# Optimization experiments

Measured on AMD Instinct MI355X. Metric: run time of the kernel, lower is better.

Reference implementation:

```python
import math
import jax, jax.numpy as jnp
import numpy as np

S, M, B, NH, HD = 512, 512, 8, 16, 64  # SentenceLength, MemoryLength, BatchSize, heads, head_size
H = NH * HD   # 1024 hidden
K = M + S     # key length = r_length
LAYERS, TOTAL_LEN = 2, 1536


def setup_inputs() -> dict:
    key = jax.random.key(0)
    ks = jax.random.split(key, 12)
    w = lambda k: jax.random.normal(k, (H, H), jnp.float32) * 0.02
    return {
        "x": jax.random.normal(ks[0], (B, S, H), jnp.float32),
        "rel_pos_emb": jax.random.normal(ks[1], (K, H), jnp.float32),
        "attention_mask": jnp.ones((B, S), jnp.float32),  # unused by the original forward
        "memories": jax.random.normal(ks[2], (LAYERS, B, TOTAL_LEN, H), jnp.float32),
        "Wq": w(ks[3]), "Wke": w(ks[4]), "Wv": w(ks[5]), "Wkr": w(ks[6]),
        "u": jax.random.normal(ks[7], (NH, HD), jnp.float32),
        "v": jax.random.normal(ks[8], (NH, HD), jnp.float32),
        "Wo": w(ks[9]),
        "bo": jnp.zeros((H,), jnp.float32),
        "layer_num": 0,
        "segment_num": 0,
    }


def rel_shift(bd):
    # Vectorized form of the original per-row loop:
    # row qi keeps bd[qi][qlen-1-qi:] and zero-pads the tail.
    qlen, klen = bd.shape[0], bd.shape[1]
    shift = (qlen - 1) - jnp.arange(qlen)            # [qlen]
    idx = shift[:, None] + jnp.arange(klen)[None, :]  # [qlen, klen]
    valid = (idx < klen)
    idx_c = jnp.minimum(idx, klen - 1)
    out = bd[jnp.arange(qlen)[:, None], idx_c]        # gather along key axis
    return out * valid[:, :, None, None].astype(bd.dtype)


def reference(x, rel_pos_emb, attention_mask, memories, Wq, Wke, Wv, Wkr, u, v, Wo, bo, layer_num, segment_num):
    # memory segment for this layer: [B, M, H]
    sg_m = memories[layer_num, :, segment_num * M:(segment_num + 1) * M, :]
    kvx = jnp.concatenate([sg_m, x], axis=1)          # [B, K, H]
    # Projections, then the original's raw .view() reinterpretation (not a transpose)
    qx = (x.reshape(-1, H) @ Wq).reshape(S, B, NH, HD)
    kx = (kvx.reshape(-1, H) @ Wke).reshape(K, B, NH, HD)
    vx = (kvx.reshape(-1, H) @ Wv).reshape(K, B, NH, HD)
    kr = (rel_pos_emb @ Wkr).reshape(K, NH, HD)
    ac = jnp.einsum('ibnd,jbnd->ijbn', qx + u, kx)    # content score [S,K,B,NH]
    bd = jnp.einsum('ibnd,jnd->ijbn', qx + v, kr)     # position score
    bd = rel_shift(bd)
    att = (ac + bd) / math.sqrt(float(HD))
    att = jax.nn.softmax(att, axis=-1)                # original uses Softmax(dim=-1) on [i,j,b,n]
    out = jnp.einsum('ijbn,jbnd->ibnd', att, vx)      # [S,B,NH,HD]
    out = out.reshape(B, S, H)                        # original's raw contiguous().view()
    out = out @ Wo + bo                               # o_dense (dropout is identity in eval)
    # update_memories_by_layer (no_grad in torch -> stop_gradient here)
    new_mem = memories.at[layer_num, :, segment_num * S + M:(segment_num + 1) * S + M, :].set(
        jax.lax.stop_gradient(out))
    return out, new_mem
```

## Files before the change

### kernel.cpp

```cpp
#include <hip/hip_runtime.h>
#include <hip/hip_bf16.h>

#define OUT_OFF 4194304
#define NM_ELEMS 25165824

typedef __attribute__((ext_vector_type(8))) short short8;
typedef __attribute__((ext_vector_type(4))) float f32x4;

static __device__ __forceinline__ float4 ld4(const float* p) {
  return *reinterpret_cast<const float4*>(p);
}
static __device__ __forceinline__ short bfbits(float f) {
  __hip_bfloat16 h = __float2bfloat16(f);
  return *reinterpret_cast<short*>(&h);
}
static __device__ __forceinline__ void gload16(const void* g, void* l) {
  __builtin_amdgcn_global_load_lds(
      (const __attribute__((address_space(1))) void*)g,
      (__attribute__((address_space(3))) void*)l, 16, 0, 0);
}

__global__ __launch_bounds__(256)
void cw_k(const float* __restrict__ W0, const float* __restrict__ W1,
          const float* __restrict__ W2, const float* __restrict__ W3,
          const float* __restrict__ W4,
          __hip_bfloat16* __restrict__ T0, __hip_bfloat16* __restrict__ T1,
          __hip_bfloat16* __restrict__ T2, __hip_bfloat16* __restrict__ T3,
          __hip_bfloat16* __restrict__ T4)
{
  const float* W; __hip_bfloat16* T;
  switch (blockIdx.z) {
    case 0: W = W0; T = T0; break;
    case 1: W = W1; T = T1; break;
    case 2: W = W2; T = T2; break;
    case 3: W = W3; T = T3; break;
    default: W = W4; T = T4; break;
  }
  __shared__ short S[64][72];
  const int t = threadIdx.x;
  const int n0 = blockIdx.x * 64, k0 = blockIdx.y * 64;
  #pragma unroll
  for (int it = 0; it < 2; ++it) {
    const int kl = (t >> 3) + it * 32;
    const int n8 = (t & 7) * 8;
    const float* src = W + (size_t)(k0 + kl) * 1024 + n0 + n8;
    const float4 f0 = ld4(src), f1 = ld4(src + 4);
    short8 s;
    s[0]=bfbits(f0.x); s[1]=bfbits(f0.y); s[2]=bfbits(f0.z); s[3]=bfbits(f0.w);
    s[4]=bfbits(f1.x); s[5]=bfbits(f1.y); s[6]=bfbits(f1.z); s[7]=bfbits(f1.w);
    *reinterpret_cast<short8*>(&S[kl][n8]) = s;
  }
  __syncthreads();
  #pragma unroll
  for (int it = 0; it < 2; ++it) {
    const int nl = (t >> 3) + it * 32;
    const int k8 = (t & 7) * 8;
    short8 s;
    #pragma unroll
    for (int e = 0; e < 8; ++e) s[e] = S[k8 + e][nl];
    *reinterpret_cast<short8*>((short*)T + (size_t)(n0 + nl) * 1024 + k0 + k8) = s;
  }
}

__global__ __launch_bounds__(256)
void ckvx_k(const float* __restrict__ x, const float* __restrict__ mem,
            const int* __restrict__ lp, const int* __restrict__ sp,
            __hip_bfloat16* __restrict__ Kvx)
{
  const size_t t = (size_t)blockIdx.x * 256 + threadIdx.x;
  const int r = (int)(t >> 7);
  const int c = (int)(t & 127) * 8;
  const int b = r >> 10, j = r & 1023;
  const float* src = (j < 512)
    ? mem + (((size_t)lp[0] * 8 + b) * 1536 + (size_t)sp[0] * 512 + j) * 1024 + c
    : x + ((size_t)b * 512 + (j - 512)) * 1024 + c;
  const float4 f0 = ld4(src), f1 = ld4(src + 4);
  short8 s;
  s[0]=bfbits(f0.x); s[1]=bfbits(f0.y); s[2]=bfbits(f0.z); s[3]=bfbits(f0.w);
  s[4]=bfbits(f1.x); s[5]=bfbits(f1.y); s[6]=bfbits(f1.z); s[7]=bfbits(f1.w);
  *reinterpret_cast<short8*>((short*)Kvx + (size_t)r * 1024 + c) = s;
}

__global__ __launch_bounds__(256)
void crpe_k(const float* __restrict__ R, __hip_bfloat16* __restrict__ Rb)
{
  const size_t t = ((size_t)blockIdx.x * 256 + threadIdx.x) * 8;
  const float4 f0 = ld4(R + t), f1 = ld4(R + t + 4);
  short8 s;
  s[0]=bfbits(f0.x); s[1]=bfbits(f0.y); s[2]=bfbits(f0.z); s[3]=bfbits(f0.w);
  s[4]=bfbits(f1.x); s[5]=bfbits(f1.y); s[6]=bfbits(f1.z); s[7]=bfbits(f1.w);
  *reinterpret_cast<short8*>((short*)Rb + t) = s;
}

template<int MODE>
__global__ __launch_bounds__(256)
void mgemm(const __hip_bfloat16* __restrict__ A,
           const __hip_bfloat16* __restrict__ Wt,
           const float* __restrict__ P0, const float* __restrict__ P1,
           const int* __restrict__ lp, const int* __restrict__ sp,
           __hip_bfloat16* __restrict__ Cb, __hip_bfloat16* __restrict__ Cb2,
           float* __restrict__ C)
{
  __shared__ __align__(16) short As[128 * 64];
  __shared__ __align__(16) short Bs[128 * 64];
  const int tid = threadIdx.x;
  const int w   = tid >> 6;
  const int l   = tid & 63;
  const int l15 = l & 15, lg = l >> 4;
  const int m0 = blockIdx.y * 128;
  const int n0 = blockIdx.x * 128;
  const int wr = (w >> 1) * 64;
  const int wc = (w & 1) * 64;

  f32x4 acc[4][4];
  #pragma unroll
  for (int mi = 0; mi < 4; ++mi)
    #pragma unroll
    for (int ni = 0; ni < 4; ++ni) acc[mi][ni] = (f32x4){0.f, 0.f, 0.f, 0.f};

  const int srow = (l >> 3);
  const int scol = (l & 7) * 8;

  for (int k0 = 0; k0 < 1024; k0 += 64) {
    if (k0) __syncthreads();
    #pragma unroll
    for (int q = 0; q < 4; ++q) {
      const int seg = w * 32 + q * 8;
      const int ra = m0 + seg + srow;
      size_t aoff;
      if (MODE == 4)
        aoff = ((size_t)(ra >> 9) * 1024 + 512 + (ra & 511)) * 1024;
      else
        aoff = (size_t)ra * 1024;
      gload16((const short*)A + aoff + k0 + scol, &As[seg * 64]);
      const int rb = n0 + seg + srow;
      gload16((const short*)Wt + (size_t)rb * 1024 + k0 + scol, &Bs[seg * 64]);
    }
    __syncthreads();
    #pragma unroll
    for (int kk = 0; kk < 2; ++kk) {
      short8 a[4], bf[4];
      #pragma unroll
      for (int mi = 0; mi < 4; ++mi)
        a[mi] = *reinterpret_cast<const short8*>(
            &As[(wr + mi * 16 + l15) * 64 + kk * 32 + lg * 8]);
      #pragma unroll
      for (int ni = 0; ni < 4; ++ni)
        bf[ni] = *reinterpret_cast<const short8*>(
            &Bs[(wc + ni * 16 + l15) * 64 + kk * 32 + lg * 8]);
      #pragma unroll
      for (int mi = 0; mi < 4; ++mi)
        #pragma unroll
        for (int ni = 0; ni < 4; ++ni)
          acc[mi][ni] = __builtin_amdgcn_mfma_f32_16x16x32_bf16(
              a[mi], bf[ni], acc[mi][ni], 0, 0, 0);
    }
  }

  #pragma unroll
  for (int mi = 0; mi < 4; ++mi) {
    const int rbase = m0 + wr + mi * 16 + lg * 4;
    #pragma unroll
    for (int ni = 0; ni < 4; ++ni) {
      const int col = n0 + wc + ni * 16 + l15;
      const int nh = col >> 6, dd = col & 63;
      #pragma unroll
      for (int rr = 0; rr < 4; ++rr) {
        const int row = rbase + rr;
        const float val = acc[mi][ni][rr];
        if (MODE == 3) {
          Cb[(size_t)row * 1024 + col] = __float2bfloat16(val);
        } else if (MODE == 4) {
          const int i = row >> 3, bb = row & 7;
          const size_t o = (((size_t)(bb * 16 + nh) * 512) + i) * 64 + dd;
          Cb [o] = __float2bfloat16(val + P0[col]);
          Cb2[o] = __float2bfloat16(val + P1[col]);
        } else if (MODE == 5) {
          const int j = row >> 3, bb = row & 7;
          Cb[(((size_t)(bb * 16 + nh) * 1024) + j) * 64 + dd] =
              __float2bfloat16(val);
        } else if (MODE == 2) {
          const float o = val + P0[col];
          C[(size_t)row * 1024 + col] = o;
          const int b2 = row >> 9, s2 = row & 511;
          C[OUT_OFF +
            (((size_t)lp[0] * 8 + b2) * 1536 + 512 + (size_t)sp[0] * 512 + s2) *
                1024 + col] = o;
        }
      }
    }
  }
}

__global__ __launch_bounds__(256)
void tr_k(const __hip_bfloat16* __restrict__ VE, __hip_bfloat16* __restrict__ Vt)
{
  __shared__ short T[64][72];
  const int t = threadIdx.x;
  const int j0 = blockIdx.x * 64;
  const int bn = blockIdx.y;
  #pragma unroll
  for (int it = 0; it < 2; ++it) {
    const int jl = (t >> 3) + it * 32;
    const int d8 = (t & 7) * 8;
    *reinterpret_cast<short8*>(&T[jl][d8]) =
        *reinterpret_cast<const short8*>(
            (const short*)VE + ((size_t)bn * 1024 + j0 + jl) * 64 + d8);
  }
  __syncthreads();
  #pragma unroll
  for (int it = 0; it < 2; ++it) {
    const int dl = (t >> 3) + it * 32;
    const int j8 = (t & 7) * 8;
    short8 s;
    #pragma unroll
    for (int e = 0; e < 8; ++e) s[e] = T[j8 + e][dl];
    *reinterpret_cast<short8*>(
        (short*)Vt + ((size_t)bn * 64 + dl) * 1024 + j0 + j8) = s;
  }
}

__global__ __launch_bounds__(512, 1)
void attn2(const __hip_bfloat16* __restrict__ QU, const __hip_bfloat16* __restrict__ QV,
           const __hip_bfloat16* __restrict__ KE, const __hip_bfloat16* __restrict__ Vt,
           const __hip_bfloat16* __restrict__ KR, __hip_bfloat16* __restrict__ Ob)
{
  __shared__ float Lbuf[16*16*33];
  __shared__ __hip_bfloat16 Abuf[16*16*36];

  const int bid = blockIdx.x;
  const int b   = bid & 7;
  const int i0  = (bid >> 3) * 16;
  const int tid = threadIdx.x;
  const int w   = tid >> 6;
  const int l   = tid & 63;
  const int l15 = l & 15;
  const int lg  = l >> 4;

  short8 qu[2][2], qv[2][2];
  #pragma unroll
  for (int hh = 0; hh < 2; ++hh) {
    const int h = 2*w + hh;
    const size_t qb = (((size_t)(b*16 + h) * 512) + i0 + l15) * 64 + lg*8;
    #pragma unroll
    for (int kf = 0; kf < 2; ++kf) {
      qu[hh][kf] = *reinterpret_cast<const short8*>(QU + qb + kf*32);
      qv[hh][kf] = *reinterpret_cast<const short8*>(QV + qb + kf*32);
    }
  }

  f32x4 oacc[2][4];
  #pragma unroll
  for (int hh = 0; hh < 2; ++hh)
    #pragma unroll
    for (int nf = 0; nf < 4; ++nf) oacc[hh][nf] = (f32x4){0.f,0.f,0.f,0.f};

  auto loadKEKR = [&](short8 (&ke)[2][2][2], short8 (&kr)[2][3][2],
                      int j0, int pb) {
    #pragma unroll
    for (int hh = 0; hh < 2; ++hh) {
      const int h = 2*w + hh;
      #pragma unroll
      for (int jf = 0; jf < 2; ++jf)
        #pragma unroll
        for (int kf = 0; kf < 2; ++kf)
          ke[hh][jf][kf] = *reinterpret_cast<const short8*>(
            KE + (((size_t)(b*16 + h) * 1024) + j0 + jf*16 + l15) * 64 + kf*32 + lg*8);
      #pragma unroll
      for (int nf = 0; nf < 3; ++nf)
        #pragma unroll
        for (int kf = 0; kf < 2; ++kf)
          kr[hh][nf][kf] = *reinterpret_cast<const short8*>(
            KR + ((size_t)(pb + nf*16 + l15)) * 1024 + h*64 + kf*32 + lg*8);
    }
  };

  auto body = [&](int jt, short8 (&keC)[2][2][2], short8 (&krC)[2][3][2],
                  short8 (&keN)[2][2][2], short8 (&krN)[2][3][2]) {
    const int j0 = jt * 32;
    const int pb = 496 - i0 + j0;

    f32x4 ac[2][2], tf[2][3];
    #pragma unroll
    for (int hh = 0; hh < 2; ++hh) {
      #pragma unroll
      for (int nf = 0; nf < 3; ++nf) {
        tf[hh][nf] = (f32x4){0,0,0,0};
        #pragma unroll
        for (int kf = 0; kf < 2; ++kf)
          tf[hh][nf] = __builtin_amdgcn_mfma_f32_16x16x32_bf16(
              qv[hh][kf], krC[hh][nf][kf], tf[hh][nf], 0, 0, 0);
      }
      #pragma unroll
      for (int jf = 0; jf < 2; ++jf) {
        ac[hh][jf] = (f32x4){0,0,0,0};
        #pragma unroll
        for (int kf = 0; kf < 2; ++kf)
          ac[hh][jf] = __builtin_amdgcn_mfma_f32_16x16x32_bf16(
              qu[hh][kf], keC[hh][jf][kf], ac[hh][jf], 0, 0, 0);
      }
    }

    loadKEKR(keN, krN, j0 + 32, pb + 32);

    short8 vb[2][4];
    #pragma unroll
    for (int hh = 0; hh < 2; ++hh) {
      const int h = 2*w + hh;
      #pragma unroll
      for (int nf = 0; nf < 4; ++nf)
        vb[hh][nf] = *reinterpret_cast<const short8*>(
          Vt + (((size_t)(b*16 + h) * 64) + nf*16 + l15) * 1024 + j0 + lg*8);
    }

    asm volatile("" ::: "memory");

    #pragma unroll
    for (int hh = 0; hh < 2; ++hh) {
      const int h = 2*w + hh;
      #pragma unroll
      for (int jf = 0; jf < 2; ++jf)
        #pragma unroll
        for (int r = 0; r < 4; ++r) {
          const int ip  = lg*4 + r;
          const int idx = 15 - ip + jf*16 + l15;
          const int nf  = idx >> 4;
          const int Ls  = lg*16 + (idx & 15);
          const float v0 = __shfl(tf[hh][0][r], Ls, 64);
          const float v1 = __shfl(tf[hh][1][r], Ls, 64);
          const float v2 = __shfl(tf[hh][2][r], Ls, 64);
          const float bd = (nf == 0) ? v0 : ((nf == 1) ? v1 : v2);
          Lbuf[(h*16 + ip)*33 + jf*16 + l15] = 0.125f * (ac[hh][jf][r] + bd);
        }
    }
    __syncthreads();

    {
      const int si = tid >> 5, sj = tid & 31;
      float vals[16];
      float m = -3.0e38f;
      #pragma unroll
      for (int n = 0; n < 16; ++n) {
        vals[n] = Lbuf[(n*16 + si)*33 + sj];
        m = fmaxf(m, vals[n]);
      }
      float s = 0.f;
      #pragma unroll
      for (int n = 0; n < 16; ++n) { vals[n] = __expf(vals[n] - m); s += vals[n]; }
      const float rinv = 1.0f / s;
      #pragma unroll
      for (int n = 0; n < 16; ++n)
        Abuf[(n*16 + si)*36 + sj] = __float2bfloat16(vals[n] * rinv);
    }
    __syncthreads();

    #pragma unroll
    for (int hh = 0; hh < 2; ++hh) {
      const int h = 2*w + hh;
      const short8 af = *reinterpret_cast<const short8*>(
          &Abuf[(h*16 + l15)*36 + lg*8]);
      #pragma unroll
      for (int nf = 0; nf < 4; ++nf)
        oacc[hh][nf] = __builtin_amdgcn_mfma_f32_16x16x32_bf16(
            af, vb[hh][nf], oacc[hh][nf], 0, 0, 0);
    }
  };

  short8 keA[2][2][2], krA[2][3][2];
  short8 keB[2][2][2], krB[2][3][2];

  loadKEKR(keA, krA, 0, 496 - i0);
  for (int jt = 0; jt < 32; jt += 2) {
    body(jt,     keA, krA, keB, krB);
    body(jt + 1, keB, krB, keA, krA);
  }

  #pragma unroll
  for (int hh = 0; hh < 2; ++hh) {
    const int h = 2*w + hh;
    #pragma unroll
    for (int nf = 0; nf < 4; ++nf)
      #pragma unroll
      for (int r = 0; r < 4; ++r) {
        const int i = i0 + lg*4 + r;
        Ob[((size_t)(i*8 + b)) * 1024 + h*64 + nf*16 + l15] =
            __float2bfloat16(oacc[hh][nf][r]);
      }
  }
}

extern "C" void kernel_launch(void* const* d_in, const int* in_sizes, int n_in,
                              void* d_out, int out_size, void* d_ws, size_t ws_size,
                              hipStream_t stream)
{
  const float* x   = (const float*)d_in[0];
  const float* rpe = (const float*)d_in[1];
  const float* mem = (const float*)d_in[3];
  const float* Wq  = (const float*)d_in[4];
  const float* Wke = (const float*)d_in[5];
  const float* Wv  = (const float*)d_in[6];
  const float* Wkr = (const float*)d_in[7];
  const float* u   = (const float*)d_in[8];
  const float* v   = (const float*)d_in[9];
  const float* Wo  = (const float*)d_in[10];
  const float* bo  = (const float*)d_in[11];
  const int* lp    = (const int*)d_in[12];
  const int* sp    = (const int*)d_in[13];

  float* out = (float*)d_out;
  float* nm  = out + OUT_OFF;

  float* ws = (float*)d_ws;
  __hip_bfloat16* QUb = (__hip_bfloat16*)(ws);
  __hip_bfloat16* QVb = (__hip_bfloat16*)(ws + 2097152);
  __hip_bfloat16* KRb = (__hip_bfloat16*)(ws + 4194304);
  __hip_bfloat16* Ob  = (__hip_bfloat16*)(ws + 4980736);
  __hip_bfloat16* Rb  = (__hip_bfloat16*)(ws + 7077888);
  __hip_bfloat16* WtO = (__hip_bfloat16*)(ws + 7602176);
  __hip_bfloat16* Kvx = (__hip_bfloat16*)(nm);
  __hip_bfloat16* KEb = (__hip_bfloat16*)(nm + 4194304);
  __hip_bfloat16* VEb = (__hip_bfloat16*)(nm + 8388608);
  __hip_bfloat16* Vtb = (__hip_bfloat16*)(nm + 12582912);
  __hip_bfloat16* WtQ = (__hip_bfloat16*)(nm + 16777216);
  __hip_bfloat16* WtK = (__hip_bfloat16*)(nm + 17301504);
  __hip_bfloat16* WtV = (__hip_bfloat16*)(nm + 17825792);
  __hip_bfloat16* WtR = (__hip_bfloat16*)(nm + 18350080);

  dim3 blk(256);
  hipMemsetAsync((void*)(KRb + (size_t)1024*1024), 0, (size_t)512*1024*2, stream);

  cw_k <<<dim3(16,16,5), blk, 0, stream>>>(Wq, Wke, Wv, Wkr, Wo,
                                           WtQ, WtK, WtV, WtR, WtO);
  ckvx_k<<<4096, blk, 0, stream>>>(x, mem, lp, sp, Kvx);
  crpe_k<<<512,  blk, 0, stream>>>(rpe, Rb);

  mgemm<3><<<dim3(8, 8),  blk, 0, stream>>>(Rb,  WtR, nullptr, nullptr, lp, sp, KRb, nullptr, nullptr);
  mgemm<4><<<dim3(8, 32), blk, 0, stream>>>(Kvx, WtQ, u, v,             lp, sp, QUb, QVb,     nullptr);
  mgemm<5><<<dim3(8, 64), blk, 0, stream>>>(Kvx, WtK, nullptr, nullptr, lp, sp, KEb, nullptr, nullptr);
  mgemm<5><<<dim3(8, 64), blk, 0, stream>>>(Kvx, WtV, nullptr, nullptr, lp, sp, VEb, nullptr, nullptr);

  tr_k<<<dim3(16, 128), blk, 0, stream>>>(VEb, Vtb);

  attn2<<<dim3(256), dim3(512), 0, stream>>>(QUb, QVb, KEb, Vtb, KRb, Ob);

  hipMemcpyAsync(nm, mem, (size_t)NM_ELEMS * 4ull, hipMemcpyDeviceToDevice, stream);

  mgemm<2><<<dim3(8, 32), blk, 0, stream>>>(Ob, WtO, bo, nullptr, lp, sp, nullptr, nullptr, out);
}
```

Baseline: 419.5 us.

## Stage KE/KR tiles through LDS with async loads and process 16-key halves

The attention kernel no longer double-buffers KE and KR fragments in registers. Each wave now copies its KE and KR tiles into a private LDS region with global_load_lds, then reads MFMA fragments from LDS. Key tiles shrink from 32 to 16 columns, so each tile needs two relative-position fragments instead of three, and the softmax and P·V step are split into two halves per 32-key block. The aim is to free registers and overlap global loads with compute. In exchange there are twice as many block barriers, half the threads sit idle during softmax, and the final prefetch reads past the end of KE/KR.

```diff
diff --git a/kernel.cpp b/kernel.cpp
--- a/kernel.cpp
+++ b/kernel.cpp
@@ -225,7 +225,8 @@
            const __hip_bfloat16* __restrict__ KE, const __hip_bfloat16* __restrict__ Vt,
            const __hip_bfloat16* __restrict__ KR, __hip_bfloat16* __restrict__ Ob)
 {
-  __shared__ float Lbuf[16*16*33];
+  __shared__ __align__(16) short stg[49152];
+  __shared__ float Lbuf[16*16*17];
   __shared__ __hip_bfloat16 Abuf[16*16*36];
 
   const int bid = blockIdx.x;
@@ -237,6 +238,12 @@
   const int l15 = l & 15;
   const int lg  = l >> 4;
 
+  short* keW = stg + w * 6144;
+  short* krW = keW + 2048;
+
+  const short* KEs = (const short*)KE;
+  const short* KRs = (const short*)KR;
+
   short8 qu[2][2], qv[2][2];
   #pragma unroll
   for (int hh = 0; hh < 2; ++hh) {
@@ -255,124 +262,129 @@
     #pragma unroll
     for (int nf = 0; nf < 4; ++nf) oacc[hh][nf] = (f32x4){0.f,0.f,0.f,0.f};
 
-  auto loadKEKR = [&](short8 (&ke)[2][2][2], short8 (&kr)[2][3][2],
-                      int j0, int pb) {
-    #pragma unroll
-    for (int hh = 0; hh < 2; ++hh) {
-      const int h = 2*w + hh;
-      #pragma unroll
-      for (int jf = 0; jf < 2; ++jf)
-        #pragma unroll
-        for (int kf = 0; kf < 2; ++kf)
-          ke[hh][jf][kf] = *reinterpret_cast<const short8*>(
-            KE + (((size_t)(b*16 + h) * 1024) + j0 + jf*16 + l15) * 64 + kf*32 + lg*8);
-      #pragma unroll
-      for (int nf = 0; nf < 3; ++nf)
-        #pragma unroll
-        for (int kf = 0; kf < 2; ++kf)
-          kr[hh][nf][kf] = *reinterpret_cast<const short8*>(
-            KR + ((size_t)(pb + nf*16 + l15)) * 1024 + h*64 + kf*32 + lg*8);
+  auto stage = [&](int j0) {
+    const int pb = 496 - i0 + j0;
+    #pragma unroll
+    for (int q = 0; q < 4; ++q) {
+      const int R  = q*8 + (l >> 3);
+      const int hh = R >> 4, jl = R & 15;
+      gload16(KEs + (((size_t)(b*16 + 2*w + hh) * 1024) + j0 + jl) * 64 + (l & 7) * 8,
+              keW + q * 512);
+    }
+    #pragma unroll
+    for (int q = 0; q < 8; ++q) {
+      const int r = q*4 + (l >> 4);
+      gload16(KRs + ((size_t)(pb + r)) * 1024 + w * 128 + (l & 15) * 8,
+              krW + q * 512);
     }
   };
 
-  auto body = [&](int jt, short8 (&keC)[2][2][2], short8 (&krC)[2][3][2],
-                  short8 (&keN)[2][2][2], short8 (&krN)[2][3][2]) {
-    const int j0 = jt * 32;
-    const int pb = 496 - i0 + j0;
-
-    f32x4 ac[2][2], tf[2][3];
-    #pragma unroll
-    for (int hh = 0; hh < 2; ++hh) {
-      #pragma unroll
-      for (int nf = 0; nf < 3; ++nf) {
-        tf[hh][nf] = (f32x4){0,0,0,0};
-        #pragma unroll
-        for (int kf = 0; kf < 2; ++kf)
-          tf[hh][nf] = __builtin_amdgcn_mfma_f32_16x16x32_bf16(
-              qv[hh][kf], krC[hh][nf][kf], tf[hh][nf], 0, 0, 0);
-      }
-      #pragma unroll
-      for (int jf = 0; jf < 2; ++jf) {
-        ac[hh][jf] = (f32x4){0,0,0,0};
-        #pragma unroll
-        for (int kf = 0; kf < 2; ++kf)
-          ac[hh][jf] = __builtin_amdgcn_mfma_f32_16x16x32_bf16(
-              qu[hh][kf], keC[hh][jf][kf], ac[hh][jf], 0, 0, 0);
-      }
-    }
-
-    loadKEKR(keN, krN, j0 + 32, pb + 32);
-
+  stage(0);
+
+  for (int pr = 0; pr < 32; ++pr) {
+    const int j0e = pr * 32;
     short8 vb[2][4];
-    #pragma unroll
-    for (int hh = 0; hh < 2; ++hh) {
-      const int h = 2*w + hh;
-      #pragma unroll
-      for (int nf = 0; nf < 4; ++nf)
-        vb[hh][nf] = *reinterpret_cast<const short8*>(
-          Vt + (((size_t)(b*16 + h) * 64) + nf*16 + l15) * 1024 + j0 + lg*8);
-    }
-
-    asm volatile("" ::: "memory");
-
-    #pragma unroll
-    for (int hh = 0; hh < 2; ++hh) {
-      const int h = 2*w + hh;
-      #pragma unroll
-      for (int jf = 0; jf < 2; ++jf)
+
+    #pragma unroll
+    for (int half = 0; half < 2; ++half) {
+      const int j0 = j0e + half * 16;
+
+      asm volatile("s_waitcnt vmcnt(0)" ::: "memory");
+      __builtin_amdgcn_sched_barrier(0);
+
+      short8 kef[2][2], krf[2][2][2];
+      #pragma unroll
+      for (int hh = 0; hh < 2; ++hh)
+        #pragma unroll
+        for (int kf = 0; kf < 2; ++kf) {
+          kef[hh][kf] = *reinterpret_cast<const short8*>(
+              keW + (hh*16 + l15)*64 + kf*32 + lg*8);
+          #pragma unroll
+          for (int nf = 0; nf < 2; ++nf)
+            krf[hh][nf][kf] = *reinterpret_cast<const short8*>(
+                krW + (nf*16 + l15)*128 + hh*64 + kf*32 + lg*8);
+        }
+
+      f32x4 ac[2], tf[2][2];
+      #pragma unroll
+      for (int hh = 0; hh < 2; ++hh) {
+        ac[hh]    = (f32x4){0,0,0,0};
+        tf[hh][0] = (f32x4){0,0,0,0};
+        tf[hh][1] = (f32x4){0,0,0,0};
+        #pragma unroll
+        for (int kf = 0; kf < 2; ++kf) {
+          ac[hh] = __builtin_amdgcn_mfma_f32_16x16x32_bf16(
+              qu[hh][kf], kef[hh][kf], ac[hh], 0, 0, 0);
+          #pragma unroll
+          for (int nf = 0; nf < 2; ++nf)
+            tf[hh][nf] = __builtin_amdgcn_mfma_f32_16x16x32_bf16(
+                qv[hh][kf], krf[hh][nf][kf], tf[hh][nf], 0, 0, 0);
+        }
+      }
+
+      asm volatile("s_waitcnt lgkmcnt(0)" ::: "memory");
+      __builtin_amdgcn_sched_barrier(0);
+      stage(j0 + 16);
+      if (half == 0) {
+        #pragma unroll
+        for (int hh = 0; hh < 2; ++hh) {
+          const int h = 2*w + hh;
+          #pragma unroll
+          for (int nf = 0; nf < 4; ++nf)
+            vb[hh][nf] = *reinterpret_cast<const short8*>(
+              Vt + (((size_t)(b*16 + h) * 64) + nf*16 + l15) * 1024 + j0e + lg*8);
+        }
+      }
+
+      #pragma unroll
+      for (int hh = 0; hh < 2; ++hh) {
+        const int h = 2*w + hh;
         #pragma unroll
         for (int r = 0; r < 4; ++r) {
           const int ip  = lg*4 + r;
-          const int idx = 15 - ip + jf*16 + l15;
+          const int idx = 15 - ip + l15;
           const int nf  = idx >> 4;
           const int Ls  = lg*16 + (idx & 15);
           const float v0 = __shfl(tf[hh][0][r], Ls, 64);
           const float v1 = __shfl(tf[hh][1][r], Ls, 64);
-          const float v2 = __shfl(tf[hh][2][r], Ls, 64);
-          const float bd = (nf == 0) ? v0 : ((nf == 1) ? v1 : v2);
-          Lbuf[(h*16 + ip)*33 + jf*16 + l15] = 0.125f * (ac[hh][jf][r] + bd);
-        }
-    }
-    __syncthreads();
-
-    {
-      const int si = tid >> 5, sj = tid & 31;
-      float vals[16];
-      float m = -3.0e38f;
-      #pragma unroll
-      for (int n = 0; n < 16; ++n) {
-        vals[n] = Lbuf[(n*16 + si)*33 + sj];
-        m = fmaxf(m, vals[n]);
-      }
-      float s = 0.f;
-      #pragma unroll
-      for (int n = 0; n < 16; ++n) { vals[n] = __expf(vals[n] - m); s += vals[n]; }
-      const float rinv = 1.0f / s;
-      #pragma unroll
-      for (int n = 0; n < 16; ++n)
-        Abuf[(n*16 + si)*36 + sj] = __float2bfloat16(vals[n] * rinv);
-    }
-    __syncthreads();
-
-    #pragma unroll
-    for (int hh = 0; hh < 2; ++hh) {
-      const int h = 2*w + hh;
-      const short8 af = *reinterpret_cast<const short8*>(
-          &Abuf[(h*16 + l15)*36 + lg*8]);
-      #pragma unroll
-      for (int nf = 0; nf < 4; ++nf)
-        oacc[hh][nf] = __builtin_amdgcn_mfma_f32_16x16x32_bf16(
-            af, vb[hh][nf], oacc[hh][nf], 0, 0, 0);
-    }
-  };
-
-  short8 keA[2][2][2], krA[2][3][2];
-  short8 keB[2][2][2], krB[2][3][2];
-
-  loadKEKR(keA, krA, 0, 496 - i0);
-  for (int jt = 0; jt < 32; jt += 2) {
-    body(jt,     keA, krA, keB, krB);
-    body(jt + 1, keB, krB, keA, krA);
+          const float bd = nf ? v1 : v0;
+          Lbuf[(h*16 + ip)*17 + l15] = 0.125f * (ac[hh][r] + bd);
+        }
+      }
+      __syncthreads();
+
+      if (tid < 256) {
+        const int si = tid >> 4, sj = tid & 15;
+        float vals[16];
+        float m = -3.0e38f;
+        #pragma unroll
+        for (int n = 0; n < 16; ++n) {
+          vals[n] = Lbuf[(n*16 + si)*17 + sj];
+          m = fmaxf(m, vals[n]);
+        }
+        float s = 0.f;
+        #pragma unroll
+        for (int n = 0; n < 16; ++n) { vals[n] = __expf(vals[n] - m); s += vals[n]; }
+        const float rinv = 1.0f / s;
+        #pragma unroll
+        for (int n = 0; n < 16; ++n)
+          Abuf[(n*16 + si)*36 + half*16 + sj] = __float2bfloat16(vals[n] * rinv);
+      }
+      __syncthreads();
+
+      if (half == 1) {
+        #pragma unroll
+        for (int hh = 0; hh < 2; ++hh) {
+          const int h = 2*w + hh;
+          const short8 af = *reinterpret_cast<const short8*>(
+              &Abuf[(h*16 + l15)*36 + lg*8]);
+          #pragma unroll
+          for (int nf = 0; nf < 4; ++nf)
+            oacc[hh][nf] = __builtin_amdgcn_mfma_f32_16x16x32_bf16(
+                af, vb[hh][nf], oacc[hh][nf], 0, 0, 0);
+        }
+      }
+    }
   }
 
   #pragma unroll
```

Result: no change. 417.6 us (-0.4%).
